# Kernel tuning notes

Hardware: AMD Instinct MI355X
Metric: run time of the kernel (lower is better)

Reference implementation:

```python
import jax, jax.numpy as jnp
import numpy as np

H = 1024
NS, NQ, S = 32, 64, 256
ADAPT_STEPS = 5


def _mlp_ln(x, W1, b1, W2, b2, g, be):
    # Linear -> ReLU -> Linear -> LayerNorm (dropout is identity in eval)
    h = jax.nn.relu(x @ W1 + b1) @ W2 + b2
    mu = h.mean(-1, keepdims=True)
    var = ((h - mu) ** 2).mean(-1, keepdims=True)
    return g * (h - mu) / jnp.sqrt(var + 1e-5) + be


def setup_inputs() -> dict:
    key = jax.random.key(0)
    ks = jax.random.split(key, 16)
    d = {}
    d['support_embeddings'] = jax.random.normal(ks[0], (NS, S, H), jnp.float32)
    d['query_embeddings'] = jax.random.normal(ks[1], (NQ, S, H), jnp.float32)
    d['support_labels'] = jax.random.randint(ks[2], (NS, S), 0, 3)
    w = lambda k, fi, fo: jax.random.normal(k, (fi, fo), jnp.float32) * (1.0 / np.sqrt(fi))
    # aspect_aware encoder
    d['aw_W1'] = w(ks[3], H, H); d['aw_b1'] = jnp.zeros((H,), jnp.float32)
    d['aw_W2'] = w(ks[4], H, H); d['aw_b2'] = jnp.zeros((H,), jnp.float32)
    d['aw_g'] = jnp.ones((H,), jnp.float32); d['aw_be'] = jnp.zeros((H,), jnp.float32)
    # aspect_contrastive encoder
    d['ct_W1'] = w(ks[5], H, H); d['ct_b1'] = jnp.zeros((H,), jnp.float32)
    d['ct_W2'] = w(ks[6], H, H); d['ct_b2'] = jnp.zeros((H,), jnp.float32)
    d['ct_g'] = jnp.ones((H,), jnp.float32); d['ct_be'] = jnp.zeros((H,), jnp.float32)
    # adaptation net (randomly-initialized 2-layer MLP in the torch code)
    d['ad_W1'] = w(ks[7], H, H); d['ad_b1'] = jnp.zeros((H,), jnp.float32)
    d['ad_W2'] = w(ks[8], H, H); d['ad_b2'] = jnp.zeros((H,), jnp.float32)
    # meta classifier
    d['cl_W1'] = w(ks[9], 2 * H, H); d['cl_b1'] = jnp.zeros((H,), jnp.float32)
    d['cl_W2'] = w(ks[10], H, 64); d['cl_b2'] = jnp.zeros((64,), jnp.float32)
    d['cl_W3'] = w(ks[11], 64, 3); d['cl_b3'] = jnp.zeros((3,), jnp.float32)
    return d


def reference(support_embeddings, query_embeddings, support_labels,
              aw_W1, aw_b1, aw_W2, aw_b2, aw_g, aw_be,
              ct_W1, ct_b1, ct_W2, ct_b2, ct_g, ct_be,
              ad_W1, ad_b1, ad_W2, ad_b2,
              cl_W1, cl_b1, cl_W2, cl_b2, cl_W3, cl_b3):
    # --- encode support set, build per-sentence aspect prototypes ---
    aw_s = _mlp_ln(support_embeddings, aw_W1, aw_b1, aw_W2, aw_b2, aw_g, aw_be)  # [NS,S,H]
    mask = (support_labels > 0).astype(aw_s.dtype)[..., None]                    # [NS,S,1]
    cnt = jnp.maximum(mask.sum(axis=1), 1.0)                                     # [NS,1]
    protos = (aw_s * mask).sum(axis=1) / cnt                                     # [NS,H] masked mean
    pn = protos / jnp.maximum(jnp.linalg.norm(protos, axis=-1, keepdims=True), 1e-8)

    # --- meta-adaptation: fused over all (query, token) pairs, 5 steps ---
    adapted = query_embeddings
    for _ in range(ADAPT_STEPS):
        qn = adapted / jnp.maximum(jnp.linalg.norm(adapted, axis=-1, keepdims=True), 1e-8)
        sims = jnp.einsum('qsh,ph->qsp', qn, pn)           # cosine similarities
        wts = jax.nn.softmax(sims, axis=-1)
        infl = jnp.einsum('qsp,ph->qsh', wts, protos)      # prototype influence
        adapted = jax.nn.relu((adapted + infl) @ ad_W1 + ad_b1) @ ad_W2 + ad_b2

    # --- classify adapted query tokens ---
    q_aw = _mlp_ln(adapted, aw_W1, aw_b1, aw_W2, aw_b2, aw_g, aw_be)
    q_ct = _mlp_ln(adapted, ct_W1, ct_b1, ct_W2, ct_b2, ct_g, ct_be)
    comb = jnp.concatenate([q_aw, q_ct], axis=-1)          # [NQ,S,2H]
    h = jax.nn.relu(comb @ cl_W1 + cl_b1)
    h = jax.nn.relu(h @ cl_W2 + cl_b2)
    preds = h @ cl_W3 + cl_b3                              # [NQ,S,3]
    return preds
```

## Files before the change

### kernel.cpp

```cpp
#include <hip/hip_runtime.h>
#include <hip/hip_bf16.h>

#define H 1024
#define NS 32
#define SS 256
#define T_Q 16384
#define M_S 8192

typedef __hip_bfloat16 bf16;
typedef short short8 __attribute__((ext_vector_type(8)));
typedef float floatx4 __attribute__((ext_vector_type(4)));

__device__ __forceinline__ float ldf(const bf16& v) { return __bfloat162float(v); }

__device__ __forceinline__ void split2(float v, bf16& h, bf16& l) {
  h = __float2bfloat16(v);
  l = __float2bfloat16(v - __bfloat162float(h));
}

__device__ __forceinline__ void gl2lds16(const void* g, void* l) {
  __builtin_amdgcn_global_load_lds(
      (const __attribute__((address_space(1))) unsigned int*)g,
      (__attribute__((address_space(3))) unsigned int*)l, 16, 0, 0);
}

__device__ __forceinline__ short8 ld8s(const bf16* p) { return *(const short8*)p; }

__global__ __launch_bounds__(256) void conv_split(const float* __restrict__ in,
                                                  bf16* __restrict__ oh,
                                                  bf16* __restrict__ ol, int n)
{
  int i = blockIdx.x * 256 + threadIdx.x;
  if (i < n) { bf16 h, l; split2(in[i], h, l); oh[i] = h; ol[i] = l; }
}

__global__ __launch_bounds__(256) void transpose_split(
    const float* __restrict__ W, bf16* __restrict__ Wh, bf16* __restrict__ Wl,
    int K, int N)
{
  __shared__ float t[32][33];
  int n0 = blockIdx.x * 32, k0 = blockIdx.y * 32;
  int tx = threadIdx.x & 31, ty = threadIdx.x >> 5;
#pragma unroll
  for (int i = 0; i < 32; i += 8)
    t[ty + i][tx] = W[(size_t)(k0 + ty + i) * N + (n0 + tx)];
  __syncthreads();
#pragma unroll
  for (int i = 0; i < 32; i += 8) {
    bf16 h, l; split2(t[tx][ty + i], h, l);
    size_t o = (size_t)(n0 + ty + i) * K + (k0 + tx);
    Wh[o] = h;
    if (Wl) Wl[o] = l;
  }
}

template<bool RELU, bool HASWL>
__global__ __launch_bounds__(512, 2) void gemm3p(
    const bf16* __restrict__ A0h, const bf16* __restrict__ A0l,
    const bf16* __restrict__ A1h, const bf16* __restrict__ A1l,
    const bf16* __restrict__ Wh,  const bf16* __restrict__ Wl,
    const float* __restrict__ bias,
    bf16* __restrict__ Ch, bf16* __restrict__ Cl,
    int M, int N, int K0, int Ktot)
{
  (void)M;
  __shared__ __align__(16) bf16 lds[2 * 32768];
  const int tid = threadIdx.x;
  const int w = tid >> 6, l = tid & 63;
  const int nbm = gridDim.x >> 2;
  const int lid = blockIdx.x;
  const int xcd = lid & 7, ib = lid >> 3;
  const int half = nbm >> 1;
  const int bn = xcd >> 1;
  const int bm = (xcd & 1) * half + ib;
  const int wr = w >> 2, wn = w & 3;
  const int m16 = l & 15, quad = l >> 4;
  const int srow = l & 15;
  const int scol = (l >> 4) * 8;

  floatx4 acc[8][4];
#pragma unroll
  for (int i = 0; i < 8; i++)
#pragma unroll
    for (int j = 0; j < 4; j++) { acc[i][j][0]=0.f; acc[i][j][1]=0.f; acc[i][j][2]=0.f; acc[i][j][3]=0.f; }

  const size_t raA0 = (size_t)(bm * 256 + (2 * w)     * 16 + srow) * H + scol;
  const size_t raA1 = (size_t)(bm * 256 + (2 * w + 1) * 16 + srow) * H + scol;
  const size_t raB0 = (size_t)(bn * 256 + (2 * w)     * 16 + srow) * Ktot + scol;
  const size_t raB1 = (size_t)(bn * 256 + (2 * w + 1) * 16 + srow) * Ktot + scol;
  const int nT = Ktot >> 5;

  auto stage = [&](int t) {
    const int k0 = t << 5;
    const bf16 *Abh, *Abl; int ke;
    if (k0 < K0) { Abh = A0h; Abl = A0l; ke = k0; }
    else         { Abh = A1h; Abl = A1l; ke = k0 - K0; }
    bf16* buf = lds + (t & 1) * 32768;
    gl2lds16(Abh + raA0 + ke, buf + (2 * w)     * 512);
    gl2lds16(Abh + raA1 + ke, buf + (2 * w + 1) * 512);
    gl2lds16(Abl + raA0 + ke, buf + 8192  + (2 * w)     * 512);
    gl2lds16(Abl + raA1 + ke, buf + 8192  + (2 * w + 1) * 512);
    gl2lds16(Wh + raB0 + k0, buf + 16384 + (2 * w)     * 512);
    gl2lds16(Wh + raB1 + k0, buf + 16384 + (2 * w + 1) * 512);
    if (HASWL) {
      gl2lds16(Wl + raB0 + k0, buf + 24576 + (2 * w)     * 512);
      gl2lds16(Wl + raB1 + k0, buf + 24576 + (2 * w + 1) * 512);
    }
  };

  stage(0);

  const int la = l * 8;
  for (int t = 0; t < nT; ++t) {
    const bf16* buf = lds + (t & 1) * 32768;
    __builtin_amdgcn_s_barrier();
    if (t + 1 < nT) {
      stage(t + 1);
      if (HASWL) asm volatile("s_waitcnt vmcnt(8)" ::: "memory");
      else       asm volatile("s_waitcnt vmcnt(6)" ::: "memory");
    } else {
      asm volatile("s_waitcnt vmcnt(0)" ::: "memory");
    }
    __builtin_amdgcn_s_barrier();

    const bf16* pA  = buf + (wr * 8) * 512 + la;
    const bf16* pAl = pA + 8192;
    const bf16* pB  = buf + 16384 + (wn * 4) * 512 + la;
    const bf16* pBl = pB + 8192;

    short8 bh[4], bl8[4];
#pragma unroll
    for (int nt = 0; nt < 4; nt++) bh[nt] = ld8s(pB + nt * 512);
    if (HASWL) {
#pragma unroll
      for (int nt = 0; nt < 4; nt++) bl8[nt] = ld8s(pBl + nt * 512);
    }

    short8 ah = ld8s(pA), al8 = ld8s(pAl);
#pragma unroll
    for (int mt = 0; mt < 8; mt++) {
      short8 nh = ah, nl = al8;
      if (mt < 7) { nh = ld8s(pA + (mt + 1) * 512); nl = ld8s(pAl + (mt + 1) * 512); }
      __builtin_amdgcn_s_setprio(1);
#pragma unroll
      for (int nt = 0; nt < 4; nt++) {
        acc[mt][nt] = __builtin_amdgcn_mfma_f32_16x16x32_bf16(ah,  bh[nt],  acc[mt][nt], 0, 0, 0);
        acc[mt][nt] = __builtin_amdgcn_mfma_f32_16x16x32_bf16(al8, bh[nt],  acc[mt][nt], 0, 0, 0);
        if (HASWL)
          acc[mt][nt] = __builtin_amdgcn_mfma_f32_16x16x32_bf16(ah, bl8[nt], acc[mt][nt], 0, 0, 0);
      }
      __builtin_amdgcn_s_setprio(0);
      ah = nh; al8 = nl;
    }
  }

#pragma unroll
  for (int mt = 0; mt < 8; mt++) {
#pragma unroll
    for (int nt = 0; nt < 4; nt++) {
      int row0 = bm * 256 + wr * 128 + mt * 16 + quad * 4;
      int col  = bn * 256 + wn * 64 + nt * 16 + m16;
      float bv = bias ? bias[col] : 0.f;
#pragma unroll
      for (int r = 0; r < 4; r++) {
        float v = acc[mt][nt][r] + bv;
        if (RELU) v = fmaxf(v, 0.f);
        bf16 h, lo; split2(v, h, lo);
        size_t o = (size_t)(row0 + r) * N + col;
        Ch[o] = h; Cl[o] = lo;
      }
    }
  }
}

__global__ __launch_bounds__(256) void ln_pair(
    bf16* __restrict__ hh, bf16* __restrict__ hl,
    const float* __restrict__ g, const float* __restrict__ be)
{
  int row = blockIdx.x;
  bf16* ph = hh + (size_t)row * H;
  bf16* pl = hl + (size_t)row * H;
  int tid = threadIdx.x;
  float v[4];
  float s = 0.f, sq = 0.f;
#pragma unroll
  for (int j = 0; j < 4; j++) {
    int hi = tid + 256 * j;
    v[j] = ldf(ph[hi]) + ldf(pl[hi]);
    s += v[j]; sq += v[j] * v[j];
  }
  __shared__ float rs[256], rq[256];
  rs[tid] = s; rq[tid] = sq; __syncthreads();
  for (int o = 128; o; o >>= 1) {
    if (tid < o) { rs[tid] += rs[tid + o]; rq[tid] += rq[tid + o]; }
    __syncthreads();
  }
  float mu   = rs[0] * (1.0f / H);
  float var  = rq[0] * (1.0f / H) - mu * mu;
  float rstd = rsqrtf(var + 1e-5f);
#pragma unroll
  for (int j = 0; j < 4; j++) {
    int hi = tid + 256 * j;
    bf16 h, l; split2(g[hi] * (v[j] - mu) * rstd + be[hi], h, l);
    ph[hi] = h; pl[hi] = l;
  }
}

__global__ __launch_bounds__(256) void proto_kernel(
    const bf16* __restrict__ eh, const bf16* __restrict__ el,
    const int* __restrict__ labels, float* __restrict__ protos_out)
{
  int p = blockIdx.x;
  int tid = threadIdx.x;
  __shared__ unsigned char lbl[SS];
  lbl[tid] = (labels[p * SS + tid] > 0) ? 1 : 0;
  __syncthreads();
  float acc[4] = {0.f, 0.f, 0.f, 0.f};
  int cnt = 0;
  const bf16* bh = eh + (size_t)p * SS * H;
  const bf16* bl = el + (size_t)p * SS * H;
  for (int s = 0; s < SS; s++) {
    if (lbl[s]) {
      cnt++;
      const bf16* rh = bh + (size_t)s * H;
      const bf16* rl = bl + (size_t)s * H;
#pragma unroll
      for (int j = 0; j < 4; j++)
        acc[j] += ldf(rh[tid + 256 * j]) + ldf(rl[tid + 256 * j]);
    }
  }
  float ic = 1.0f / fmaxf((float)cnt, 1.0f);
#pragma unroll
  for (int j = 0; j < 4; j++) protos_out[p * H + tid + 256 * j] = acc[j] * ic;
}

__global__ __launch_bounds__(256) void pn_kernel(
    const float* __restrict__ protos, bf16* __restrict__ pnh, bf16* __restrict__ pnl)
{
  int p = blockIdx.x;
  int tid = threadIdx.x;
  __shared__ float red[256];
  float v[4];
  float sq = 0.f;
#pragma unroll
  for (int j = 0; j < 4; j++) { v[j] = protos[p * H + tid + 256 * j]; sq += v[j] * v[j]; }
  red[tid] = sq; __syncthreads();
  for (int o = 128; o; o >>= 1) {
    if (tid < o) red[tid] += red[tid + o];
    __syncthreads();
  }
  float inv = 1.0f / fmaxf(sqrtf(red[0]), 1e-8f);
#pragma unroll
  for (int j = 0; j < 4; j++) {
    bf16 h, l; split2(v[j] * inv, h, l);
    pnh[p * H + tid + 256 * j] = h;
    pnl[p * H + tid + 256 * j] = l;
  }
}

__global__ __launch_bounds__(256) void rownorm_pair(
    const bf16* __restrict__ hh, const bf16* __restrict__ hl, float* __restrict__ rn)
{
  int row = blockIdx.x;
  int tid = threadIdx.x;
  const bf16* ph = hh + (size_t)row * H;
  const bf16* pl = hl + (size_t)row * H;
  float s = 0.f;
#pragma unroll
  for (int j = 0; j < 4; j++) {
    float v = ldf(ph[tid + 256 * j]) + ldf(pl[tid + 256 * j]);
    s += v * v;
  }
  __shared__ float rs[256];
  rs[tid] = s; __syncthreads();
  for (int o = 128; o; o >>= 1) {
    if (tid < o) rs[tid] += rs[tid + o];
    __syncthreads();
  }
  if (tid == 0) rn[row] = 1.0f / fmaxf(sqrtf(rs[0]), 1e-8f);
}

__global__ __launch_bounds__(256) void sims_mfma(
    const bf16* __restrict__ Ah, const bf16* __restrict__ Al,
    const bf16* __restrict__ Bh, const bf16* __restrict__ Bl,
    float* __restrict__ sims)
{
  __shared__ bf16 AsH[64 * 32];
  __shared__ bf16 AsL[64 * 32];
  __shared__ bf16 BsH[32 * 32];
  __shared__ bf16 BsL[32 * 32];
  const int tid = threadIdx.x;
  const int w = tid >> 6, l = tid & 63;
  const int bm0 = blockIdx.x * 64;
  const int m16 = l & 15, quad = l >> 4;
  const int sr = l >> 2;
  const int sc = (l & 3) * 8;

  floatx4 acc[2];
#pragma unroll
  for (int nt = 0; nt < 2; nt++) { acc[nt][0]=0.f; acc[nt][1]=0.f; acc[nt][2]=0.f; acc[nt][3]=0.f; }

  for (int k0 = 0; k0 < H; k0 += 32) {
    gl2lds16(Ah + (size_t)(bm0 + w * 16 + sr) * H + k0 + sc, &AsH[w * 512]);
    gl2lds16(Al + (size_t)(bm0 + w * 16 + sr) * H + k0 + sc, &AsL[w * 512]);
    if (w < 2) gl2lds16(Bh + (size_t)(w * 16 + sr) * H + k0 + sc, &BsH[w * 512]);
    else       gl2lds16(Bl + (size_t)((w - 2) * 16 + sr) * H + k0 + sc, &BsL[(w - 2) * 512]);
    __syncthreads();

    short8 ah  = *(const short8*)&AsH[(w * 16 + m16) * 32 + quad * 8];
    short8 al8 = *(const short8*)&AsL[(w * 16 + m16) * 32 + quad * 8];
#pragma unroll
    for (int nt = 0; nt < 2; nt++) {
      short8 bh  = *(const short8*)&BsH[(nt * 16 + m16) * 32 + quad * 8];
      short8 bl8 = *(const short8*)&BsL[(nt * 16 + m16) * 32 + quad * 8];
      acc[nt] = __builtin_amdgcn_mfma_f32_16x16x32_bf16(ah,  bh,  acc[nt], 0, 0, 0);
      acc[nt] = __builtin_amdgcn_mfma_f32_16x16x32_bf16(al8, bh,  acc[nt], 0, 0, 0);
      acc[nt] = __builtin_amdgcn_mfma_f32_16x16x32_bf16(ah,  bl8, acc[nt], 0, 0, 0);
    }
    __syncthreads();
  }

#pragma unroll
  for (int nt = 0; nt < 2; nt++) {
    int col  = nt * 16 + m16;
    int row0 = bm0 + w * 16 + quad * 4;
#pragma unroll
    for (int r = 0; r < 4; r++)
      sims[(size_t)(row0 + r) * 32 + col] = acc[nt][r];
  }
}

__global__ __launch_bounds__(256) void softmax32(
    const float* __restrict__ sims, const float* __restrict__ rn,
    float* __restrict__ wts)
{
  int t = blockIdx.x * 8 + (threadIdx.x >> 5);
  int p = threadIdx.x & 31;
  float s = sims[(size_t)t * 32 + p] * rn[t];
  float m = s;
#pragma unroll
  for (int o = 16; o; o >>= 1) m = fmaxf(m, __shfl_xor(m, o, 64));
  float e = __expf(s - m);
  float sum = e;
#pragma unroll
  for (int o = 16; o; o >>= 1) sum += __shfl_xor(sum, o, 64);
  wts[(size_t)t * 32 + p] = e / sum;
}

__global__ __launch_bounds__(256) void infl16(
    const bf16* __restrict__ ah, const bf16* __restrict__ al,
    const float* __restrict__ wts, const float* __restrict__ protos,
    bf16* __restrict__ oh, bf16* __restrict__ ol)
{
  int t0 = blockIdx.x * 16;
  int tid = threadIdx.x;
  __shared__ float wl[16][32];
  for (int i = tid; i < 512; i += 256)
    wl[i >> 5][i & 31] = wts[(size_t)(t0 + (i >> 5)) * 32 + (i & 31)];
  __syncthreads();
  int c0 = tid * 4;
  float acc[16][4];
#pragma unroll
  for (int tk = 0; tk < 16; tk++) {
    const bf16* rh = ah + (size_t)(t0 + tk) * H + c0;
    const bf16* rl = al + (size_t)(t0 + tk) * H + c0;
#pragma unroll
    for (int j = 0; j < 4; j++) acc[tk][j] = ldf(rh[j]) + ldf(rl[j]);
  }
  for (int p = 0; p < 32; p++) {
    float4 pv = *(const float4*)&protos[p * H + c0];
#pragma unroll
    for (int tk = 0; tk < 16; tk++) {
      float w = wl[tk][p];
      acc[tk][0] += w * pv.x; acc[tk][1] += w * pv.y;
      acc[tk][2] += w * pv.z; acc[tk][3] += w * pv.w;
    }
  }
#pragma unroll
  for (int tk = 0; tk < 16; tk++) {
    bf16* wh = oh + (size_t)(t0 + tk) * H + c0;
    bf16* wo = ol + (size_t)(t0 + tk) * H + c0;
#pragma unroll
    for (int j = 0; j < 4; j++) { bf16 h, lo; split2(acc[tk][j], h, lo); wh[j] = h; wo[j] = lo; }
  }
}

__global__ __launch_bounds__(256) void gemm_small(
    const bf16* __restrict__ Ah, const bf16* __restrict__ Al,
    const float* __restrict__ W, const float* __restrict__ bias,
    float* __restrict__ C, int M, int N, int K)
{
  const int BK = 16;
  __shared__ float As[BK][64];
  __shared__ float Bs[BK][64];
  int tid = threadIdx.x;
  int tx = tid & 15, ty = tid >> 4;
  int bn0 = blockIdx.x * 64;
  int bm0 = blockIdx.y * 64;
  float acc[4][4] = {};
  int am = tid >> 2, ak = (tid & 3) * 4;
  int bk = tid >> 4, bn = (tid & 15) * 4;
  const bf16* Aph = Ah + (size_t)(bm0 + am) * K + ak;
  const bf16* Apl = Al + (size_t)(bm0 + am) * K + ak;
  const float* Wptr = W + (size_t)bk * N + bn0 + bn;
  for (int k0 = 0; k0 < K; k0 += BK) {
#pragma unroll
    for (int c = 0; c < 4; c++) As[ak + c][am] = ldf(Aph[c]) + ldf(Apl[c]);
#pragma unroll
    for (int c = 0; c < 4; c++) Bs[bk][bn + c] = Wptr[c];
    __syncthreads();
#pragma unroll
    for (int k = 0; k < BK; k++) {
      float a[4], b[4];
#pragma unroll
      for (int i = 0; i < 4; i++) a[i] = As[k][ty * 4 + i];
#pragma unroll
      for (int j = 0; j < 4; j++) b[j] = Bs[k][tx * 4 + j];
#pragma unroll
      for (int i = 0; i < 4; i++)
#pragma unroll
        for (int j = 0; j < 4; j++)
          acc[i][j] += a[i] * b[j];
    }
    __syncthreads();
    Aph += BK; Apl += BK;
    Wptr += (size_t)BK * N;
  }
#pragma unroll
  for (int i = 0; i < 4; i++) {
    float* Crow = C + (size_t)(bm0 + ty * 4 + i) * N + bn0;
#pragma unroll
    for (int j = 0; j < 4; j++) {
      int n = tx * 4 + j;
      Crow[n] = fmaxf(acc[i][j] + bias[bn0 + n], 0.f);
    }
  }
}

__global__ __launch_bounds__(256) void FewShotABSALearner_46935402610855_kernel(
    const float* __restrict__ h2, const float* __restrict__ W3,
    const float* __restrict__ b3, float* __restrict__ out,
    int t0, int nElem, int out_size)
{
  int idx = blockIdx.x * 256 + threadIdx.x;
  if (idx >= nElem) return;
  int t = idx / 3, c = idx - t * 3;
  float acc = b3[c];
  const float* hr = h2 + (size_t)t * 64;
#pragma unroll
  for (int k = 0; k < 64; k++) acc += hr[k] * W3[k * 3 + c];
  int oi = t0 * 3 + idx;
  if (oi < out_size) out[oi] = acc;
}

extern "C" void kernel_launch(void* const* d_in, const int* in_sizes, int n_in,
                              void* d_out, int out_size, void* d_ws, size_t ws_size,
                              hipStream_t stream)
{
  (void)in_sizes; (void)n_in;
  const float* sup   = (const float*)d_in[0];
  const float* qry   = (const float*)d_in[1];
  const int*   lab   = (const int*)d_in[2];
  const float *aw_W1 = (const float*)d_in[3],  *aw_b1 = (const float*)d_in[4];
  const float *aw_W2 = (const float*)d_in[5],  *aw_b2 = (const float*)d_in[6];
  const float *aw_g  = (const float*)d_in[7],  *aw_be = (const float*)d_in[8];
  const float *ct_W1 = (const float*)d_in[9],  *ct_b1 = (const float*)d_in[10];
  const float *ct_W2 = (const float*)d_in[11], *ct_b2 = (const float*)d_in[12];
  const float *ct_g  = (const float*)d_in[13], *ct_be = (const float*)d_in[14];
  const float *ad_W1 = (const float*)d_in[15], *ad_b1 = (const float*)d_in[16];
  const float *ad_W2 = (const float*)d_in[17], *ad_b2 = (const float*)d_in[18];
  const float *cl_W1 = (const float*)d_in[19], *cl_b1 = (const float*)d_in[20];
  const float *cl_W2 = (const float*)d_in[21], *cl_b2 = (const float*)d_in[22];
  const float *cl_W3 = (const float*)d_in[23], *cl_b3 = (const float*)d_in[24];
  float* out = (float*)d_out;

  const size_t MB = 1 << 20;
  int C; bool clLo = true;
  if      (ws_size >= (size_t)239403008) C = 16384;
  else if (ws_size >= (size_t)136609792) C = 8192;
  else if (ws_size >= (size_t)85213184)  C = 4096;
  else if (ws_size >= (size_t)59514880)  C = 2048;
  else if (ws_size >= (size_t)46665728)  C = 1024;
  else { C = 1024; clLo = false; }
  const int Cs = (C < M_S) ? C : M_S;
  const size_t actB = (size_t)C * H * sizeof(bf16);

  char* ws = (char*)d_ws;
  size_t off = 0;
  auto nxt = [&](size_t b) { char* p = ws + off; off += b; return p; };
  bf16* sqw[12];
  for (int i = 0; i < 12; i++) sqw[i] = (bf16*)nxt(2 * MB);
  bf16 *aw1h = sqw[0], *aw1l = sqw[1], *aw2h = sqw[2],  *aw2l = sqw[3];
  bf16 *ct1h = sqw[4], *ct1l = sqw[5], *ct2h = sqw[6],  *ct2l = sqw[7];
  bf16 *ad1h = sqw[8], *ad1l = sqw[9], *ad2h = sqw[10], *ad2l = sqw[11];
  bf16* clW1h = (bf16*)nxt(4 * MB);
  bf16* clW1l = clLo ? (bf16*)nxt(4 * MB) : nullptr;
  float* protos = (float*)nxt(NS * H * 4);
  bf16*  pnh    = (bf16*)nxt(NS * H * 2);
  bf16*  pnl    = (bf16*)nxt(NS * H * 2);
  char*  ub     = nxt((size_t)C * 256);
  float* h2c   = (float*)ub;
  float* simsb = (float*)ub;
  float* wtsb  = (float*)(ub + (size_t)C * 128);
  float* rn    = (float*)nxt((size_t)C * 4);
  bf16 *R0h = (bf16*)nxt(actB), *R0l = (bf16*)nxt(actB);
  bf16 *R1h = (bf16*)nxt(actB), *R1l = (bf16*)nxt(actB);
  bf16 *R2h = (bf16*)nxt(actB), *R2l = (bf16*)nxt(actB);

  dim3 blk(256);
  dim3 blk2(512);
  dim3 tg(32, 32);
  dim3 ggq((C / 256) * 4);
  dim3 ggs((Cs / 256) * 4);

  transpose_split<<<tg, blk, 0, stream>>>(aw_W1, aw1h, aw1l, H, H);
  transpose_split<<<tg, blk, 0, stream>>>(aw_W2, aw2h, aw2l, H, H);
  transpose_split<<<tg, blk, 0, stream>>>(ct_W1, ct1h, ct1l, H, H);
  transpose_split<<<tg, blk, 0, stream>>>(ct_W2, ct2h, ct2l, H, H);
  transpose_split<<<tg, blk, 0, stream>>>(ad_W1, ad1h, ad1l, H, H);
  transpose_split<<<tg, blk, 0, stream>>>(ad_W2, ad2h, ad2l, H, H);
  transpose_split<<<dim3(32, 64), blk, 0, stream>>>(cl_W1, clW1h, clW1l, 2 * H, H);

  for (int sc = 0; sc < M_S / Cs; sc++) {
    conv_split<<<(Cs * H) / 256, blk, 0, stream>>>(sup + (size_t)sc * Cs * H, R0h, R0l, Cs * H);
    gemm3p<true , true><<<ggs, blk2, 0, stream>>>(R0h, R0l, R0h, R0l, aw1h, aw1l, aw_b1, R1h, R1l, Cs, H, H, H);
    gemm3p<false, true><<<ggs, blk2, 0, stream>>>(R1h, R1l, R1h, R1l, aw2h, aw2l, aw_b2, R2h, R2l, Cs, H, H, H);
    ln_pair<<<Cs, blk, 0, stream>>>(R2h, R2l, aw_g, aw_be);
    proto_kernel<<<Cs / SS, blk, 0, stream>>>(R2h, R2l, lab + sc * Cs,
                                              protos + (size_t)sc * (Cs / SS) * H);
  }
  pn_kernel<<<NS, blk, 0, stream>>>(protos, pnh, pnl);

  for (int qc = 0; qc < T_Q / C; qc++) {
    const float* q0 = qry + (size_t)qc * C * H;
    conv_split<<<(C * H) / 256, blk, 0, stream>>>(q0, R2h, R2l, C * H);
    for (int it = 0; it < 5; it++) {
      rownorm_pair<<<C, blk, 0, stream>>>(R2h, R2l, rn);
      sims_mfma<<<C / 64, blk, 0, stream>>>(R2h, R2l, pnh, pnl, simsb);
      softmax32<<<C / 8, blk, 0, stream>>>(simsb, rn, wtsb);
      infl16<<<C / 16, blk, 0, stream>>>(R2h, R2l, wtsb, protos, R0h, R0l);
      gemm3p<true , true><<<ggq, blk2, 0, stream>>>(R0h, R0l, R0h, R0l, ad1h, ad1l, ad_b1, R1h, R1l, C, H, H, H);
      gemm3p<false, true><<<ggq, blk2, 0, stream>>>(R1h, R1l, R1h, R1l, ad2h, ad2l, ad_b2, R2h, R2l, C, H, H, H);
    }
    gemm3p<true , true><<<ggq, blk2, 0, stream>>>(R2h, R2l, R2h, R2l, aw1h, aw1l, aw_b1, R0h, R0l, C, H, H, H);
    gemm3p<false, true><<<ggq, blk2, 0, stream>>>(R0h, R0l, R0h, R0l, aw2h, aw2l, aw_b2, R1h, R1l, C, H, H, H);
    ln_pair<<<C, blk, 0, stream>>>(R1h, R1l, aw_g, aw_be);
    gemm3p<true , true><<<ggq, blk2, 0, stream>>>(R2h, R2l, R2h, R2l, ct1h, ct1l, ct_b1, R0h, R0l, C, H, H, H);
    gemm3p<false, true><<<ggq, blk2, 0, stream>>>(R0h, R0l, R0h, R0l, ct2h, ct2l, ct_b2, R2h, R2l, C, H, H, H);
    ln_pair<<<C, blk, 0, stream>>>(R2h, R2l, ct_g, ct_be);
    if (clLo)
      gemm3p<true, true ><<<ggq, blk2, 0, stream>>>(R1h, R1l, R2h, R2l, clW1h, clW1l, cl_b1, R0h, R0l, C, H, H, 2 * H);
    else
      gemm3p<true, false><<<ggq, blk2, 0, stream>>>(R1h, R1l, R2h, R2l, clW1h, nullptr, cl_b1, R0h, R0l, C, H, H, 2 * H);
    gemm_small<<<dim3(1, C / 64), blk, 0, stream>>>(R0h, R0l, cl_W2, cl_b2, h2c, C, 64, H);
    FewShotABSALearner_46935402610855_kernel<<<(C * 3 + 255) / 256, blk, 0, stream>>>(
        h2c, cl_W3, cl_b3, out, qc * C, C * 3, out_size);
  }
}
```

Measured before the change: 2.629 ms.

## Split GEMM k-loop into barrier-phased stages with staggered next-tile prefetch

Restructures the split-bf16 MFMA GEMM main loop into four phases of two M-tiles each, separated by barriers. Global-to-LDS prefetch of the next k-tile is split in two. The B tiles and the A tiles needed first are issued in the first phase, and the remaining A tiles are issued in the second phase. Wait counts are tuned so the first phase of the next iteration can begin before the whole tile has landed. The goal is to overlap memory latency with MFMA work and smooth LDS/VMEM traffic. The cost is many more barriers per iteration and more fragile vmcnt bookkeeping.

```diff
diff --git a/kernel.cpp b/kernel.cpp
--- a/kernel.cpp
+++ b/kernel.cpp
@@ -84,75 +84,125 @@
 #pragma unroll
     for (int j = 0; j < 4; j++) { acc[i][j][0]=0.f; acc[i][j][1]=0.f; acc[i][j][2]=0.f; acc[i][j][3]=0.f; }
 
-  const size_t raA0 = (size_t)(bm * 256 + (2 * w)     * 16 + srow) * H + scol;
-  const size_t raA1 = (size_t)(bm * 256 + (2 * w + 1) * 16 + srow) * H + scol;
   const size_t raB0 = (size_t)(bn * 256 + (2 * w)     * 16 + srow) * Ktot + scol;
   const size_t raB1 = (size_t)(bn * 256 + (2 * w + 1) * 16 + srow) * Ktot + scol;
-  const int nT = Ktot >> 5;
-
-  auto stage = [&](int t) {
+  const int aT  = ((w >> 1) & 1) + ((w >> 1) >> 1) * 8;
+  const int aLo = w & 1;
+  const size_t raA = (size_t)(bm * 256 + aT * 16 + srow) * H + scol;
+  const int aDst = (aLo ? 8192 : 0) + aT * 512;
+  size_t raBt[3]; int bDst[3]; int bLo[3];
+#pragma unroll
+  for (int i = 0; i < 3; i++) {
+    int j = w * 3 + i;
+    int idx = j >> 1;
+    int tb = (idx < 6) ? (idx + 2) : (idx + 4);
+    bLo[i] = j & 1;
+    raBt[i] = (size_t)(bm * 256 + tb * 16 + srow) * H + scol;
+    bDst[i] = (bLo[i] ? 8192 : 0) + tb * 512;
+  }
+
+  auto stage_alpha = [&](int t) {
     const int k0 = t << 5;
-    const bf16 *Abh, *Abl; int ke;
-    if (k0 < K0) { Abh = A0h; Abl = A0l; ke = k0; }
-    else         { Abh = A1h; Abl = A1l; ke = k0 - K0; }
+    const bf16 *Ah_, *Al_; int ke;
+    if (k0 < K0) { Ah_ = A0h; Al_ = A0l; ke = k0; }
+    else         { Ah_ = A1h; Al_ = A1l; ke = k0 - K0; }
     bf16* buf = lds + (t & 1) * 32768;
-    gl2lds16(Abh + raA0 + ke, buf + (2 * w)     * 512);
-    gl2lds16(Abh + raA1 + ke, buf + (2 * w + 1) * 512);
-    gl2lds16(Abl + raA0 + ke, buf + 8192  + (2 * w)     * 512);
-    gl2lds16(Abl + raA1 + ke, buf + 8192  + (2 * w + 1) * 512);
-    gl2lds16(Wh + raB0 + k0, buf + 16384 + (2 * w)     * 512);
+    gl2lds16(Wh + raB0 + k0, buf + 16384 + (2 * w) * 512);
     gl2lds16(Wh + raB1 + k0, buf + 16384 + (2 * w + 1) * 512);
     if (HASWL) {
-      gl2lds16(Wl + raB0 + k0, buf + 24576 + (2 * w)     * 512);
+      gl2lds16(Wl + raB0 + k0, buf + 24576 + (2 * w) * 512);
       gl2lds16(Wl + raB1 + k0, buf + 24576 + (2 * w + 1) * 512);
     }
+    gl2lds16((aLo ? Al_ : Ah_) + raA + ke, buf + aDst);
   };
-
-  stage(0);
+  auto stage_beta = [&](int t) {
+    const int k0 = t << 5;
+    const bf16 *Ah_, *Al_; int ke;
+    if (k0 < K0) { Ah_ = A0h; Al_ = A0l; ke = k0; }
+    else         { Ah_ = A1h; Al_ = A1l; ke = k0 - K0; }
+    bf16* buf = lds + (t & 1) * 32768;
+#pragma unroll
+    for (int i = 0; i < 3; i++)
+      gl2lds16((bLo[i] ? Al_ : Ah_) + raBt[i] + ke, buf + bDst[i]);
+  };
+
+  stage_alpha(0);
+  stage_beta(0);
+  asm volatile("s_waitcnt vmcnt(3)" ::: "memory");
+  __builtin_amdgcn_s_barrier();
 
   const int la = l * 8;
+  const int nT = Ktot >> 5;
+
+#define MM3(MI, AH, AL)                                                                            \
+    _Pragma("unroll")                                                                              \
+    for (int nt = 0; nt < 4; nt++) {                                                               \
+      acc[MI][nt] = __builtin_amdgcn_mfma_f32_16x16x32_bf16(AH, bh[nt],  acc[MI][nt], 0, 0, 0);    \
+      acc[MI][nt] = __builtin_amdgcn_mfma_f32_16x16x32_bf16(AL, bh[nt],  acc[MI][nt], 0, 0, 0);    \
+      if (HASWL)                                                                                   \
+        acc[MI][nt] = __builtin_amdgcn_mfma_f32_16x16x32_bf16(AH, bl8[nt], acc[MI][nt], 0, 0, 0);  \
+    }
+
   for (int t = 0; t < nT; ++t) {
-    const bf16* buf = lds + (t & 1) * 32768;
-    __builtin_amdgcn_s_barrier();
+    bf16* buf = lds + (t & 1) * 32768;
+    const bf16* bA  = buf + (wr * 8) * 512 + la;
+    const bf16* bAl = bA + 8192;
+    const bf16* bB  = buf + 16384 + (wn * 4) * 512 + la;
+    const bf16* bBl = bB + 8192;
+
+    short8 bh[4], bl8[4];
+#pragma unroll
+    for (int nt = 0; nt < 4; nt++) bh[nt] = ld8s(bB + nt * 512);
+    if (HASWL) {
+#pragma unroll
+      for (int nt = 0; nt < 4; nt++) bl8[nt] = ld8s(bBl + nt * 512);
+    }
+    short8 a0h = ld8s(bA),       a0l = ld8s(bAl);
+    short8 a1h = ld8s(bA + 512), a1l = ld8s(bAl + 512);
+    if (t + 1 < nT) stage_alpha(t + 1);
+    __builtin_amdgcn_s_barrier();
+    __builtin_amdgcn_s_setprio(1);
+    MM3(0, a0h, a0l)
+    MM3(1, a1h, a1l)
+    __builtin_amdgcn_s_setprio(0);
     if (t + 1 < nT) {
-      stage(t + 1);
-      if (HASWL) asm volatile("s_waitcnt vmcnt(8)" ::: "memory");
-      else       asm volatile("s_waitcnt vmcnt(6)" ::: "memory");
+      if (HASWL) asm volatile("s_waitcnt vmcnt(5)" ::: "memory");
+      else       asm volatile("s_waitcnt vmcnt(3)" ::: "memory");
     } else {
       asm volatile("s_waitcnt vmcnt(0)" ::: "memory");
     }
     __builtin_amdgcn_s_barrier();
 
-    const bf16* pA  = buf + (wr * 8) * 512 + la;
-    const bf16* pAl = pA + 8192;
-    const bf16* pB  = buf + 16384 + (wn * 4) * 512 + la;
-    const bf16* pBl = pB + 8192;
-
-    short8 bh[4], bl8[4];
-#pragma unroll
-    for (int nt = 0; nt < 4; nt++) bh[nt] = ld8s(pB + nt * 512);
-    if (HASWL) {
-#pragma unroll
-      for (int nt = 0; nt < 4; nt++) bl8[nt] = ld8s(pBl + nt * 512);
-    }
-
-    short8 ah = ld8s(pA), al8 = ld8s(pAl);
-#pragma unroll
-    for (int mt = 0; mt < 8; mt++) {
-      short8 nh = ah, nl = al8;
-      if (mt < 7) { nh = ld8s(pA + (mt + 1) * 512); nl = ld8s(pAl + (mt + 1) * 512); }
-      __builtin_amdgcn_s_setprio(1);
-#pragma unroll
-      for (int nt = 0; nt < 4; nt++) {
-        acc[mt][nt] = __builtin_amdgcn_mfma_f32_16x16x32_bf16(ah,  bh[nt],  acc[mt][nt], 0, 0, 0);
-        acc[mt][nt] = __builtin_amdgcn_mfma_f32_16x16x32_bf16(al8, bh[nt],  acc[mt][nt], 0, 0, 0);
-        if (HASWL)
-          acc[mt][nt] = __builtin_amdgcn_mfma_f32_16x16x32_bf16(ah, bl8[nt], acc[mt][nt], 0, 0, 0);
-      }
-      __builtin_amdgcn_s_setprio(0);
-      ah = nh; al8 = nl;
-    }
-  }
+    short8 a2h = ld8s(bA + 1024), a2l = ld8s(bAl + 1024);
+    short8 a3h = ld8s(bA + 1536), a3l = ld8s(bAl + 1536);
+    if (t + 1 < nT) stage_beta(t + 1);
+    __builtin_amdgcn_s_barrier();
+    __builtin_amdgcn_s_setprio(1);
+    MM3(2, a2h, a2l)
+    MM3(3, a3h, a3l)
+    __builtin_amdgcn_s_setprio(0);
+    __builtin_amdgcn_s_barrier();
+
+    short8 a4h = ld8s(bA + 2048), a4l = ld8s(bAl + 2048);
+    short8 a5h = ld8s(bA + 2560), a5l = ld8s(bAl + 2560);
+    __builtin_amdgcn_s_barrier();
+    __builtin_amdgcn_s_setprio(1);
+    MM3(4, a4h, a4l)
+    MM3(5, a5h, a5l)
+    __builtin_amdgcn_s_setprio(0);
+    __builtin_amdgcn_s_barrier();
+
+    short8 a6h = ld8s(bA + 3072), a6l = ld8s(bAl + 3072);
+    short8 a7h = ld8s(bA + 3584), a7l = ld8s(bAl + 3584);
+    __builtin_amdgcn_s_barrier();
+    __builtin_amdgcn_s_setprio(1);
+    MM3(6, a6h, a6l)
+    MM3(7, a7h, a7l)
+    __builtin_amdgcn_s_setprio(0);
+    if (t + 1 < nT) asm volatile("s_waitcnt vmcnt(3)" ::: "memory");
+    __builtin_amdgcn_s_barrier();
+  }
+#undef MM3
 
 #pragma unroll
   for (int mt = 0; mt < 8; mt++) {
```

Measured after the change: 2.484 ms. -5.5%, faster.

## Switch GEMM to 32x32x16 MFMA with staged ping-pong load/compute schedule

Applied to the files above, without the earlier changes.

Replaces the 16x16x32 MFMA tiling with 32x32x16 MFMA tiles (4x2 per wave) and changes the LDS layout to 32-row slabs. The main loop is split into four compute phases, with the next tile's weight and activation global-to-LDS copies and the LDS fragment reads interleaved between them and separated by barriers. The aim is to hide LDS and global latency behind MFMA work and to use the larger, more efficient MFMA shape. The cost is more live fragment registers and more barriers per K step. The output index mapping now follows the 32x32 accumulator layout, which is a correctness risk if any part of that mapping is wrong.

```diff
diff --git a/kernel.cpp b/kernel.cpp
--- a/kernel.cpp
+++ b/kernel.cpp
@@ -10,6 +10,7 @@
 typedef __hip_bfloat16 bf16;
 typedef short short8 __attribute__((ext_vector_type(8)));
 typedef float floatx4 __attribute__((ext_vector_type(4)));
+typedef float floatx16 __attribute__((ext_vector_type(16)));
 
 __device__ __forceinline__ float ldf(const bf16& v) { return __bfloat162float(v); }
 
@@ -74,99 +75,136 @@
   const int bn = xcd >> 1;
   const int bm = (xcd & 1) * half + ib;
   const int wr = w >> 2, wn = w & 3;
-  const int m16 = l & 15, quad = l >> 4;
-  const int srow = l & 15;
-  const int scol = (l >> 4) * 8;
-
-  floatx4 acc[8][4];
-#pragma unroll
-  for (int i = 0; i < 8; i++)
-#pragma unroll
-    for (int j = 0; j < 4; j++) { acc[i][j][0]=0.f; acc[i][j][1]=0.f; acc[i][j][2]=0.f; acc[i][j][3]=0.f; }
-
-  const size_t raA0 = (size_t)(bm * 256 + (2 * w)     * 16 + srow) * H + scol;
-  const size_t raA1 = (size_t)(bm * 256 + (2 * w + 1) * 16 + srow) * H + scol;
-  const size_t raB0 = (size_t)(bn * 256 + (2 * w)     * 16 + srow) * Ktot + scol;
-  const size_t raB1 = (size_t)(bn * 256 + (2 * w + 1) * 16 + srow) * Ktot + scol;
+  const int srow = l & 31;
+  const int scol = (l >> 5) * 8;
+  const int la = l * 8;
+
+  floatx16 acc[4][2];
+#pragma unroll
+  for (int i = 0; i < 4; i++)
+#pragma unroll
+    for (int j = 0; j < 2; j++)
+#pragma unroll
+      for (int r = 0; r < 16; r++) acc[i][j][r] = 0.f;
+
+  const size_t raB = (size_t)(bn * 256 + w * 32 + srow) * Ktot + scol;
+  const size_t raA = (size_t)(bm * 256 + w * 32 + srow) * H + scol;
+
+  auto stage_alpha = [&](int t) {
+    const int k0 = t << 5;
+    bf16* buf = lds + (t & 1) * 32768;
+    gl2lds16(Wh + raB + k0,      buf + 16384 + (w * 2 + 0) * 512);
+    gl2lds16(Wh + raB + k0 + 16, buf + 16384 + (w * 2 + 1) * 512);
+    if (HASWL) {
+      gl2lds16(Wl + raB + k0,      buf + 24576 + (w * 2 + 0) * 512);
+      gl2lds16(Wl + raB + k0 + 16, buf + 24576 + (w * 2 + 1) * 512);
+    }
+  };
+  auto stage_beta = [&](int t) {
+    const int k0 = t << 5;
+    const bf16 *Ah_, *Al_; int ke;
+    if (k0 < K0) { Ah_ = A0h; Al_ = A0l; ke = k0; }
+    else         { Ah_ = A1h; Al_ = A1l; ke = k0 - K0; }
+    bf16* buf = lds + (t & 1) * 32768;
+    gl2lds16(Ah_ + raA + ke,      buf + (w * 2 + 0) * 512);
+    gl2lds16(Ah_ + raA + ke + 16, buf + (w * 2 + 1) * 512);
+    gl2lds16(Al_ + raA + ke,      buf + 8192 + (w * 2 + 0) * 512);
+    gl2lds16(Al_ + raA + ke + 16, buf + 8192 + (w * 2 + 1) * 512);
+  };
+
+  const int aoff = wr * 4096 + la;
+  const int boff = 16384 + wn * 2048 + la;
+
+  stage_alpha(0);
+  stage_beta(0);
+  asm volatile("s_waitcnt vmcnt(0)" ::: "memory");
+  __builtin_amdgcn_s_barrier();
+
+  short8 A0f[2], A0g[2], A1f[2], A1g[2], A2f[2], A2g[2], A3f[2], A3g[2];
+  short8 B0f[2], B0g[2], B1f[2], B1g[2];
+  {
+    const bf16* buf = lds;
+    B0f[0] = ld8s(buf + boff);          B0f[1] = ld8s(buf + boff + 1024);
+    if (HASWL) { B0g[0] = ld8s(buf + boff + 8192); B0g[1] = ld8s(buf + boff + 9216); }
+    A0f[0] = ld8s(buf + aoff);          A0f[1] = ld8s(buf + aoff + 1024);
+    A0g[0] = ld8s(buf + aoff + 8192);   A0g[1] = ld8s(buf + aoff + 9216);
+  }
+
   const int nT = Ktot >> 5;
 
-  auto stage = [&](int t) {
-    const int k0 = t << 5;
-    const bf16 *Abh, *Abl; int ke;
-    if (k0 < K0) { Abh = A0h; Abl = A0l; ke = k0; }
-    else         { Abh = A1h; Abl = A1l; ke = k0 - K0; }
-    bf16* buf = lds + (t & 1) * 32768;
-    gl2lds16(Abh + raA0 + ke, buf + (2 * w)     * 512);
-    gl2lds16(Abh + raA1 + ke, buf + (2 * w + 1) * 512);
-    gl2lds16(Abl + raA0 + ke, buf + 8192  + (2 * w)     * 512);
-    gl2lds16(Abl + raA1 + ke, buf + 8192  + (2 * w + 1) * 512);
-    gl2lds16(Wh + raB0 + k0, buf + 16384 + (2 * w)     * 512);
-    gl2lds16(Wh + raB1 + k0, buf + 16384 + (2 * w + 1) * 512);
-    if (HASWL) {
-      gl2lds16(Wl + raB0 + k0, buf + 24576 + (2 * w)     * 512);
-      gl2lds16(Wl + raB1 + k0, buf + 24576 + (2 * w + 1) * 512);
-    }
-  };
-
-  stage(0);
-
-  const int la = l * 8;
+#define CL(ACC, AH, AL, BH, BL)                                                       \
+    ACC = __builtin_amdgcn_mfma_f32_32x32x16_bf16(AH, BH, ACC, 0, 0, 0);              \
+    ACC = __builtin_amdgcn_mfma_f32_32x32x16_bf16(AL, BH, ACC, 0, 0, 0);              \
+    if (HASWL) ACC = __builtin_amdgcn_mfma_f32_32x32x16_bf16(AH, BL, ACC, 0, 0, 0);
+
   for (int t = 0; t < nT; ++t) {
-    const bf16* buf = lds + (t & 1) * 32768;
+    const bf16* buf  = lds + (t & 1) * 32768;
+    const bf16* nbuf = lds + ((t + 1) & 1) * 32768;
+
+    if (t + 1 < nT) stage_alpha(t + 1);
+    A1f[0] = ld8s(buf + aoff + 2048);  A1f[1] = ld8s(buf + aoff + 3072);
+    A1g[0] = ld8s(buf + aoff + 10240); A1g[1] = ld8s(buf + aoff + 11264);
+    B1f[0] = ld8s(buf + boff + 512);   B1f[1] = ld8s(buf + boff + 1536);
+    if (HASWL) { B1g[0] = ld8s(buf + boff + 8704); B1g[1] = ld8s(buf + boff + 9728); }
+    __builtin_amdgcn_s_setprio(1);
+    CL(acc[0][0], A0f[0], A0g[0], B0f[0], B0g[0])
+    CL(acc[0][1], A0f[0], A0g[0], B0f[1], B0g[1])
+    CL(acc[1][0], A0f[1], A0g[1], B0f[0], B0g[0])
+    CL(acc[1][1], A0f[1], A0g[1], B0f[1], B0g[1])
+    __builtin_amdgcn_s_setprio(0);
     __builtin_amdgcn_s_barrier();
+
+    if (t + 1 < nT) stage_beta(t + 1);
+    A2f[0] = ld8s(buf + aoff + 512);   A2f[1] = ld8s(buf + aoff + 1536);
+    A2g[0] = ld8s(buf + aoff + 8704);  A2g[1] = ld8s(buf + aoff + 9728);
+    __builtin_amdgcn_s_setprio(1);
+    CL(acc[2][0], A1f[0], A1g[0], B0f[0], B0g[0])
+    CL(acc[2][1], A1f[0], A1g[0], B0f[1], B0g[1])
+    CL(acc[3][0], A1f[1], A1g[1], B0f[0], B0g[0])
+    CL(acc[3][1], A1f[1], A1g[1], B0f[1], B0g[1])
+    __builtin_amdgcn_s_setprio(0);
+    __builtin_amdgcn_s_barrier();
+
+    A3f[0] = ld8s(buf + aoff + 2560);  A3f[1] = ld8s(buf + aoff + 3584);
+    A3g[0] = ld8s(buf + aoff + 10752); A3g[1] = ld8s(buf + aoff + 11776);
+    __builtin_amdgcn_s_setprio(1);
+    CL(acc[0][0], A2f[0], A2g[0], B1f[0], B1g[0])
+    CL(acc[0][1], A2f[0], A2g[0], B1f[1], B1g[1])
+    CL(acc[1][0], A2f[1], A2g[1], B1f[0], B1g[0])
+    CL(acc[1][1], A2f[1], A2g[1], B1f[1], B1g[1])
+    __builtin_amdgcn_s_setprio(0);
+    asm volatile("s_waitcnt vmcnt(0)" ::: "memory");
+    __builtin_amdgcn_s_barrier();
+
     if (t + 1 < nT) {
-      stage(t + 1);
-      if (HASWL) asm volatile("s_waitcnt vmcnt(8)" ::: "memory");
-      else       asm volatile("s_waitcnt vmcnt(6)" ::: "memory");
-    } else {
-      asm volatile("s_waitcnt vmcnt(0)" ::: "memory");
-    }
-    __builtin_amdgcn_s_barrier();
-
-    const bf16* pA  = buf + (wr * 8) * 512 + la;
-    const bf16* pAl = pA + 8192;
-    const bf16* pB  = buf + 16384 + (wn * 4) * 512 + la;
-    const bf16* pBl = pB + 8192;
-
-    short8 bh[4], bl8[4];
-#pragma unroll
-    for (int nt = 0; nt < 4; nt++) bh[nt] = ld8s(pB + nt * 512);
-    if (HASWL) {
-#pragma unroll
-      for (int nt = 0; nt < 4; nt++) bl8[nt] = ld8s(pBl + nt * 512);
-    }
-
-    short8 ah = ld8s(pA), al8 = ld8s(pAl);
-#pragma unroll
-    for (int mt = 0; mt < 8; mt++) {
-      short8 nh = ah, nl = al8;
-      if (mt < 7) { nh = ld8s(pA + (mt + 1) * 512); nl = ld8s(pAl + (mt + 1) * 512); }
-      __builtin_amdgcn_s_setprio(1);
-#pragma unroll
-      for (int nt = 0; nt < 4; nt++) {
-        acc[mt][nt] = __builtin_amdgcn_mfma_f32_16x16x32_bf16(ah,  bh[nt],  acc[mt][nt], 0, 0, 0);
-        acc[mt][nt] = __builtin_amdgcn_mfma_f32_16x16x32_bf16(al8, bh[nt],  acc[mt][nt], 0, 0, 0);
-        if (HASWL)
-          acc[mt][nt] = __builtin_amdgcn_mfma_f32_16x16x32_bf16(ah, bl8[nt], acc[mt][nt], 0, 0, 0);
-      }
-      __builtin_amdgcn_s_setprio(0);
-      ah = nh; al8 = nl;
-    }
-  }
-
-#pragma unroll
-  for (int mt = 0; mt < 8; mt++) {
-#pragma unroll
-    for (int nt = 0; nt < 4; nt++) {
-      int row0 = bm * 256 + wr * 128 + mt * 16 + quad * 4;
-      int col  = bn * 256 + wn * 64 + nt * 16 + m16;
+      B0f[0] = ld8s(nbuf + boff);          B0f[1] = ld8s(nbuf + boff + 1024);
+      if (HASWL) { B0g[0] = ld8s(nbuf + boff + 8192); B0g[1] = ld8s(nbuf + boff + 9216); }
+      A0f[0] = ld8s(nbuf + aoff);          A0f[1] = ld8s(nbuf + aoff + 1024);
+      A0g[0] = ld8s(nbuf + aoff + 8192);   A0g[1] = ld8s(nbuf + aoff + 9216);
+    }
+    __builtin_amdgcn_s_setprio(1);
+    CL(acc[2][0], A3f[0], A3g[0], B1f[0], B1g[0])
+    CL(acc[2][1], A3f[0], A3g[0], B1f[1], B1g[1])
+    CL(acc[3][0], A3f[1], A3g[1], B1f[0], B1g[0])
+    CL(acc[3][1], A3f[1], A3g[1], B1f[1], B1g[1])
+    __builtin_amdgcn_s_setprio(0);
+  }
+#undef CL
+
+#pragma unroll
+  for (int mt = 0; mt < 4; mt++) {
+#pragma unroll
+    for (int nt = 0; nt < 2; nt++) {
+      int col  = bn * 256 + wn * 64 + nt * 32 + (l & 31);
+      int row0 = bm * 256 + wr * 128 + mt * 32 + 4 * (l >> 5);
       float bv = bias ? bias[col] : 0.f;
 #pragma unroll
-      for (int r = 0; r < 4; r++) {
+      for (int r = 0; r < 16; r++) {
+        int row = row0 + (r & 3) + 8 * (r >> 2);
         float v = acc[mt][nt][r] + bv;
         if (RELU) v = fmaxf(v, 0.f);
         bf16 h, lo; split2(v, h, lo);
-        size_t o = (size_t)(row0 + r) * N + col;
+        size_t o = (size_t)row * N + col;
         Ch[o] = h; Cl[o] = lo;
       }
     }
```

New measurement: 2.658 ms. No clear change (+1.1%).
